# Optimization experiments

Measured on AMD Instinct MI355X. Metric: run time of the kernel, lower is better.

## Reference

```python
import jax, jax.numpy as jnp
import numpy as np

D_MODEL = 1024
NUM_HEADS = 16


def setup_inputs() -> dict:
    key = jax.random.key(0)
    ks = jax.random.split(key, 5)
    std = float(np.sqrt(2.0 / (D_MODEL + D_MODEL)))
    def w(k):
        # approximate trunc_normal init with clipped normal (init only; math of fwd unaffected)
        v = jax.random.truncated_normal(k, -3.0, 3.0, (D_MODEL, D_MODEL), jnp.float32) * std
        return v
    x = jax.random.normal(ks[0], (4, 2048, D_MODEL), jnp.float32)
    return {
        "x": x,
        "wq": w(ks[1]),
        "wk": w(ks[2]),
        "wv": w(ks[3]),
        "wo": w(ks[4]),
    }


def reference(x, wq, wk, wv, wo):
    b, s, d = x.shape
    h = NUM_HEADS
    dk = d // h
    # Linear: einsum('o i, ... i -> ... o')
    def proj(w):
        y = jnp.einsum('oi,bsi->bso', w, x)
        return y.reshape(b, s, h, dk).transpose(0, 2, 1, 3)  # b h s dk
    Q, K, V = proj(wq), proj(wk), proj(wv)
    scale = 1.0 / jnp.sqrt(jnp.asarray(dk, x.dtype))
    scores = jnp.einsum('bhqd,bhkd->bhqk', Q, K) * scale
    mask = jnp.tril(jnp.ones((s, s), dtype=bool))
    scores = jnp.where(mask, scores, -jnp.inf)
    attn = jax.nn.softmax(scores, axis=-1)
    out = jnp.einsum('bhqk,bhkd->bhqd', attn, V)
    out = out.transpose(0, 2, 1, 3).reshape(b, s, d)
    return jnp.einsum('oi,bsi->bso', wo, out)
```

## Files before the change

### kernel.cpp

```cpp
#include <hip/hip_runtime.h>
#include <hip/hip_bf16.h>


typedef __bf16 bf16x8 __attribute__((ext_vector_type(8)));
typedef __bf16 bf16x4 __attribute__((ext_vector_type(4)));
typedef float  f32x4  __attribute__((ext_vector_type(4)));
typedef float  f32x16 __attribute__((ext_vector_type(16)));
typedef unsigned int u32x4_t __attribute__((ext_vector_type(4)));

#define GLOBAL_AS __attribute__((address_space(1)))
#define LDS_AS    __attribute__((address_space(3)))

__device__ __forceinline__ void gload16(const void* g, void* l) {
    __builtin_amdgcn_global_load_lds((const GLOBAL_AS void*)g, (LDS_AS void*)l, 16, 0, 0);
}

__device__ __forceinline__ unsigned int cvtpk_bf16(float lo, float hi) {
    unsigned int r;
    asm("v_cvt_pk_bf16_f32 %0, %1, %2" : "=v"(r) : "v"(lo), "v"(hi));
    return r;
}

#define WAITVM4 asm volatile("s_waitcnt vmcnt(4)" ::: "memory")
#define WAITVM0 asm volatile("s_waitcnt vmcnt(0)" ::: "memory")
#define WAITLGKM0 asm volatile("s_waitcnt lgkmcnt(0)" ::: "memory")
#define SCHEDB  __builtin_amdgcn_sched_barrier(0)

__global__ __launch_bounds__(256) void cast_kernel(
    const float* __restrict__ x, const float* __restrict__ wq,
    const float* __restrict__ wk, const float* __restrict__ wv,
    const float* __restrict__ wo, __bf16* __restrict__ xb, __bf16* __restrict__ wb) {
    int bid = blockIdx.x;
    const float* src; __bf16* dst; int base;
    if (bid < 4096) {
        src = x; dst = xb; base = bid * 2048;
    } else {
        int r = bid - 4096; int wi = r >> 9;
        src = (wi == 0) ? wq : (wi == 1) ? wk : (wi == 2) ? wv : wo;
        dst = wb + wi * 1048576; base = (r & 511) * 2048;
    }
    int idx = base + threadIdx.x * 8;
    float4 a = *(const float4*)(src + idx);
    float4 b = *(const float4*)(src + idx + 4);
    bf16x8 o;
    o[0] = (__bf16)a.x; o[1] = (__bf16)a.y; o[2] = (__bf16)a.z; o[3] = (__bf16)a.w;
    o[4] = (__bf16)b.x; o[5] = (__bf16)b.y; o[6] = (__bf16)b.z; o[7] = (__bf16)b.w;
    *(bf16x8*)(dst + idx) = o;
}

__global__ __launch_bounds__(512) void gemm_qkv_kernel(
    const __bf16* __restrict__ A, const __bf16* __restrict__ W,
    __bf16* __restrict__ Qb, __bf16* __restrict__ Kb, __bf16* __restrict__ Vt,
    float qscale) {
    __shared__ __align__(16) char lds[131072];
    const int t = threadIdx.x;
    const int wid = t >> 6, lane = t & 63;
    const int g = lane >> 4, m = lane & 15;
    const int wm = wid >> 2, wn = wid & 3;
    const int bid = (blockIdx.x & 7) * 48 + (blockIdx.x >> 3);
    const int mt = bid / 12, nt = bid % 12;
    const int m0 = mt * 256, n0 = nt * 256;
    const bool isV = (n0 >= 2048);

    const __bf16* aSrc[2][2]; int aDst[2][2];
    const __bf16* bSrc[2][2]; int bDst[2][2];
#pragma unroll
    for (int q = 0; q < 2; ++q) {
        const int j = t + q * 512;
        const int slot = j & 7;
        {
            const int r0 = (j >> 9) * 128 + ((j >> 3) & 63);
            aSrc[0][q] = A + (size_t)(m0 + r0) * 1024 + (slot ^ (r0 & 7)) * 8;
            aDst[0][q] = r0 * 128 + slot * 16;
            const int r1 = r0 + 64;
            aSrc[1][q] = A + (size_t)(m0 + r1) * 1024 + (slot ^ (r1 & 7)) * 8;
            aDst[1][q] = r1 * 128 + slot * 16;
        }
        {
            const int r0 = ((j >> 8) & 3) * 64 + ((j >> 3) & 31);
            bSrc[0][q] = W + (size_t)(n0 + r0) * 1024 + (slot ^ (r0 & 7)) * 8;
            bDst[0][q] = r0 * 128 + slot * 16;
            const int r1 = r0 + 32;
            bSrc[1][q] = W + (size_t)(n0 + r1) * 1024 + (slot ^ (r1 & 7)) * 8;
            bDst[1][q] = r1 * 128 + slot * 16;
        }
    }
    auto stageA = [&](int par, int kt, int d) {
        gload16(aSrc[par][0] + kt * 64, lds + d * 65536 + aDst[par][0]);
        gload16(aSrc[par][1] + kt * 64, lds + d * 65536 + aDst[par][1]);
    };
    auto stageB = [&](int par, int kt, int d) {
        gload16(bSrc[par][0] + kt * 64, lds + d * 65536 + 32768 + bDst[par][0]);
        gload16(bSrc[par][1] + kt * 64, lds + d * 65536 + 32768 + bDst[par][1]);
    };

    const int sw = (m & 7) << 4;
    const int offA0 = (wm * 128 + m) * 128 + ((g << 4) ^ sw);
    const int offB0 = (wn * 64 + m) * 128 + ((g << 4) ^ sw);

    stageA(0, 0, 0); stageA(1, 0, 0); stageB(0, 0, 0); stageB(1, 0, 0);
    stageA(0, 1, 1); stageB(0, 1, 1);
    WAITVM4;
    SCHEDB;
    __builtin_amdgcn_s_barrier();
    SCHEDB;

    f32x4 acc[8][4] = {};

#define QPHASE(MH, NH, STAGESTMT, POSTW)                                      \
    {                                                                         \
        const char* bA_ = lds + bufd * 65536;                                 \
        const char* bB_ = bA_ + 32768;                                        \
        bf16x8 af[4][2], bfr[2][2];                                           \
        _Pragma("unroll")                                                     \
        for (int i2 = 0; i2 < 4; ++i2) {                                      \
            const int off = offA0 + ((MH) * 4 + i2) * 2048;                   \
            af[i2][0] = *(const bf16x8*)(bA_ + off);                          \
            af[i2][1] = *(const bf16x8*)(bA_ + (off ^ 64));                   \
        }                                                                     \
        _Pragma("unroll")                                                     \
        for (int j2 = 0; j2 < 2; ++j2) {                                      \
            const int off = offB0 + ((NH) * 2 + j2) * 2048;                   \
            bfr[j2][0] = *(const bf16x8*)(bB_ + off);                         \
            bfr[j2][1] = *(const bf16x8*)(bB_ + (off ^ 64));                  \
        }                                                                     \
        STAGESTMT;                                                            \
        SCHEDB;                                                               \
        __builtin_amdgcn_s_barrier();                                         \
        WAITLGKM0; SCHEDB;                                                    \
        __builtin_amdgcn_s_setprio(1);                                        \
        if (isV) {                                                            \
            _Pragma("unroll")                                                 \
            for (int i2 = 0; i2 < 4; ++i2)                                    \
                _Pragma("unroll")                                             \
                for (int j2 = 0; j2 < 2; ++j2) {                              \
                    acc[(MH)*4+i2][(NH)*2+j2] = __builtin_amdgcn_mfma_f32_16x16x32_bf16( \
                        af[i2][0], bfr[j2][0], acc[(MH)*4+i2][(NH)*2+j2], 0, 0, 0);      \
                    acc[(MH)*4+i2][(NH)*2+j2] = __builtin_amdgcn_mfma_f32_16x16x32_bf16( \
                        af[i2][1], bfr[j2][1], acc[(MH)*4+i2][(NH)*2+j2], 0, 0, 0);      \
                }                                                             \
        } else {                                                              \
            _Pragma("unroll")                                                 \
            for (int i2 = 0; i2 < 4; ++i2)                                    \
                _Pragma("unroll")                                             \
                for (int j2 = 0; j2 < 2; ++j2) {                              \
                    acc[(MH)*4+i2][(NH)*2+j2] = __builtin_amdgcn_mfma_f32_16x16x32_bf16( \
                        bfr[j2][0], af[i2][0], acc[(MH)*4+i2][(NH)*2+j2], 0, 0, 0);      \
                    acc[(MH)*4+i2][(NH)*2+j2] = __builtin_amdgcn_mfma_f32_16x16x32_bf16( \
                        bfr[j2][1], af[i2][1], acc[(MH)*4+i2][(NH)*2+j2], 0, 0, 0);      \
                }                                                             \
        }                                                                     \
        __builtin_amdgcn_s_setprio(0);                                        \
        POSTW;                                                                \
        SCHEDB;                                                               \
        __builtin_amdgcn_s_barrier();                                         \
        SCHEDB;                                                               \
    }

    for (int kt = 0; kt < 16; ++kt) {
        const int bufd = kt & 1;
        const int nb = bufd ^ 1;
        QPHASE(0, 0, if (kt + 1 < 16) stageA(1, kt + 1, nb), );
        QPHASE(0, 1, if (kt + 1 < 16) stageB(1, kt + 1, nb), );
        QPHASE(1, 0, if (kt + 2 < 16) stageA(0, kt + 2, bufd), );
        if (kt < 14) {
            QPHASE(1, 1, stageB(0, kt + 2, bufd), WAITVM4);
        } else {
            QPHASE(1, 1, , WAITVM0);
        }
    }
#undef QPHASE

    if (isV) {
        const int bb = m0 >> 11;
        const int sb = (m0 & 2047) + wm * 128 + 4 * g;
        const int hbase = ((n0 - 2048) >> 6) + wn;
#pragma unroll
        for (int mi = 0; mi < 8; ++mi)
#pragma unroll
            for (int ni = 0; ni < 4; ++ni) {
                const int d = ni * 16 + m;
                bf16x4 pk;
                pk[0] = (__bf16)(acc[mi][ni][0]); pk[1] = (__bf16)(acc[mi][ni][1]);
                pk[2] = (__bf16)(acc[mi][ni][2]); pk[3] = (__bf16)(acc[mi][ni][3]);
                *(bf16x4*)(Vt + ((size_t)(bb * 16 + hbase) * 64 + d) * 2048 + sb + mi * 16) = pk;
            }
    } else {
        __bf16* C = (n0 < 1024) ? Qb : Kb;
        const float sc = (n0 < 1024) ? qscale : 1.f;
        const int cb = (n0 & 1023) + wn * 64 + 4 * g;
        const int row = m0 + wm * 128 + m;
#pragma unroll
        for (int mi = 0; mi < 8; ++mi)
#pragma unroll
            for (int ni = 0; ni < 4; ++ni) {
                bf16x4 pk;
                pk[0] = (__bf16)(acc[mi][ni][0] * sc); pk[1] = (__bf16)(acc[mi][ni][1] * sc);
                pk[2] = (__bf16)(acc[mi][ni][2] * sc); pk[3] = (__bf16)(acc[mi][ni][3] * sc);
                *(bf16x4*)(C + (size_t)(row + mi * 16) * 1024 + cb + ni * 16) = pk;
            }
    }
}

__global__ __launch_bounds__(256) void gemm_out_kernel(
    const __bf16* __restrict__ A, const __bf16* __restrict__ W, float* __restrict__ out) {
    __shared__ __align__(16) char lds[65536];
    const int t = threadIdx.x;
    const int wid = t >> 6, lane = t & 63;
    const int g = lane >> 4, m = lane & 15;
    const int wm = wid >> 1, wn = wid & 1;
    const int bid = (blockIdx.x & 7) * 64 + (blockIdx.x >> 3);
    const int mt = bid >> 3, nt = bid & 7;
    const int m0 = mt * 128, n0 = nt * 128;

    const __bf16* sA[4]; const __bf16* sB[4]; int dA[4];
#pragma unroll
    for (int i = 0; i < 4; ++i) {
        const int ci = i * 256 + t;
        const int row = ci >> 3;
        const int k8 = (ci & 7) ^ (row & 7);
        sA[i] = A + (size_t)(m0 + row) * 1024 + k8 * 8;
        sB[i] = W + (size_t)(n0 + row) * 1024 + k8 * 8;
        dA[i] = ci * 16;
    }
    auto stage = [&](int kt, char* buf) {
#pragma unroll
        for (int i = 0; i < 4; ++i) gload16(sA[i] + kt * 64, buf + dA[i]);
#pragma unroll
        for (int i = 0; i < 4; ++i) gload16(sB[i] + kt * 64, buf + 16384 + dA[i]);
    };

    const int sw = (m & 7) << 4;
    const int offA = (wm * 64 + m) * 128 + ((g << 4) ^ sw);
    const int offB = (wn * 64 + m) * 128 + ((g << 4) ^ sw);

    stage(0, lds);

    f32x4 acc[4][4] = {};
    for (int kt = 0; kt < 16; ++kt) {
        char* cbuf = lds + (kt & 1) * 32768;
        WAITVM0;
        SCHEDB;
        __builtin_amdgcn_s_barrier();
        SCHEDB;
        if (kt < 15) stage(kt + 1, lds + ((kt + 1) & 1) * 32768);
        const char* bA = cbuf;
        const char* bB = cbuf + 16384;
        bf16x8 a0[4], b0[4], a1[4], b1[4];
#pragma unroll
        for (int i = 0; i < 4; ++i) {
            a0[i] = *(const bf16x8*)(bA + (offA + i * 2048));
            b0[i] = *(const bf16x8*)(bB + (offB + i * 2048));
            a1[i] = *(const bf16x8*)(bA + ((offA + i * 2048) ^ 64));
            b1[i] = *(const bf16x8*)(bB + ((offB + i * 2048) ^ 64));
        }
        __builtin_amdgcn_s_setprio(1);
#pragma unroll
        for (int mi = 0; mi < 4; ++mi)
#pragma unroll
            for (int ni = 0; ni < 4; ++ni)
                acc[mi][ni] = __builtin_amdgcn_mfma_f32_16x16x32_bf16(b0[ni], a0[mi], acc[mi][ni], 0, 0, 0);
#pragma unroll
        for (int mi = 0; mi < 4; ++mi)
#pragma unroll
            for (int ni = 0; ni < 4; ++ni)
                acc[mi][ni] = __builtin_amdgcn_mfma_f32_16x16x32_bf16(b1[ni], a1[mi], acc[mi][ni], 0, 0, 0);
        __builtin_amdgcn_s_setprio(0);
    }

    const int row = m0 + wm * 64 + m;
    const int col = n0 + wn * 64 + 4 * g;
#pragma unroll
    for (int mi = 0; mi < 4; ++mi)
#pragma unroll
        for (int ni = 0; ni < 4; ++ni)
            *(f32x4*)(out + (size_t)(row + mi * 16) * 1024 + col + ni * 16) = acc[mi][ni];
}

__global__ __launch_bounds__(128, 2) void attn_kernel(
    const __bf16* __restrict__ Qb, const __bf16* __restrict__ Kb,
    const __bf16* __restrict__ Vt, __bf16* __restrict__ Ob) {
    __shared__ __align__(16) char lds[32768];
    const int t = threadIdx.x;
    const int w = t >> 6, lane = t & 63;
    const int l31 = lane & 31, hi = lane >> 5;
    const int qb = (blockIdx.x >> 3) & 15;
    const int bh = (blockIdx.x & 7) | ((blockIdx.x >> 7) << 3);
    const size_t sbase = (size_t)(bh >> 4) * 2048;
    const int hoff = (bh & 15) * 64;

    const char* Kbase = (const char*)Kb + (sbase * 1024 + hoff) * 2;
    const char* Vbase = (const char*)Vt + (size_t)bh * 262144;
    const int srow = lane >> 3;
    const int scol = ((lane & 7) ^ srow) << 4;
    const int sw = (l31 & 7) << 4;
    int colx[4];
#pragma unroll
    for (int i = 0; i < 4; ++i) colx[i] = (32 * i + 16 * hi) ^ sw;

    auto stage = [&](int kv0, char* lK) {
        char* lV = lK + 8192;
#pragma unroll
        for (int i = 0; i < 4; ++i) {
            const int chunk = i * 2 + w;
            const int row = chunk * 8 + srow;
            gload16(Kbase + (size_t)(kv0 + row) * 2048 + scol, lK + chunk * 1024);
            gload16(Vbase + (size_t)row * 4096 + (size_t)kv0 * 2 + scol, lV + chunk * 1024);
        }
    };

    const int q0A = qb * 64 + w * 32;
    const int q0B = (31 - qb) * 64 + w * 32;
    const int qA = q0A + l31, qB = q0B + l31;
    const int nstream = 32 - qb;

    const __bf16* qrowA = Qb + (sbase + q0A + l31) * 1024 + hoff + 8 * hi;
    const __bf16* qrowB = Qb + (sbase + q0B + l31) * 1024 + hoff + 8 * hi;
    bf16x8 qfA[4], qfB[4];
#pragma unroll
    for (int cq = 0; cq < 4; ++cq) {
        qfA[cq] = *(const bf16x8*)(qrowA + 16 * cq);
        qfB[cq] = *(const bf16x8*)(qrowB + 16 * cq);
    }

    f32x16 oA0 = {}, oA1 = {}, oB0 = {}, oB1 = {};
    float mA = -__builtin_inff(), lA = 0.f;
    float mB = -__builtin_inff(), lB = 0.f;

    auto process = [&](const f32x16& s0r, const f32x16& s1r, int qq, bool diag,
                       int kv0, float& mrun, float& lrun, f32x16& o0, f32x16& o1,
                       const char* lV) {
        float pp[32];
#pragma unroll
        for (int rr = 0; rr < 16; ++rr) { pp[rr] = s0r[rr]; pp[16 + rr] = s1r[rr]; }
        if (diag) {
#pragma unroll
            for (int rr = 0; rr < 16; ++rr) {
                const int kvl = (rr & 3) + 8 * (rr >> 2) + 4 * hi;
                if (kv0 + kvl > qq)      pp[rr]      = -__builtin_inff();
                if (kv0 + 32 + kvl > qq) pp[16 + rr] = -__builtin_inff();
            }
        }
        float m8[8];
#pragma unroll
        for (int i = 0; i < 8; ++i)
            m8[i] = fmaxf(fmaxf(pp[4 * i], pp[4 * i + 1]), fmaxf(pp[4 * i + 2], pp[4 * i + 3]));
        float tmax = fmaxf(fmaxf(fmaxf(m8[0], m8[1]), fmaxf(m8[2], m8[3])),
                           fmaxf(fmaxf(m8[4], m8[5]), fmaxf(m8[6], m8[7])));
        const bool skip = __all(tmax <= mrun + 8.f);
        if (!skip) {
            float tq = fmaxf(tmax, __shfl_xor(tmax, 32));
            float mnew = fmaxf(mrun, tq);
            float al = __builtin_amdgcn_exp2f(mrun - mnew);
            lrun *= al;
#pragma unroll
            for (int rr = 0; rr < 16; ++rr) { o0[rr] *= al; o1[rr] *= al; }
            mrun = mnew;
        }
#pragma unroll
        for (int rr = 0; rr < 32; ++rr) pp[rr] = __builtin_amdgcn_exp2f(pp[rr] - mrun);
        float s8[8];
#pragma unroll
        for (int i = 0; i < 8; ++i)
            s8[i] = (pp[4 * i] + pp[4 * i + 1]) + (pp[4 * i + 2] + pp[4 * i + 3]);
        float rsum = ((s8[0] + s8[1]) + (s8[2] + s8[3])) + ((s8[4] + s8[5]) + (s8[6] + s8[7]));
        rsum += __shfl_xor(rsum, 32);
        lrun += rsum;

        __builtin_amdgcn_s_setprio(1);
#pragma unroll
        for (int cc = 0; cc < 4; ++cc) {
            const int pb = cc * 8;
            unsigned int A0 = cvtpk_bf16(pp[pb + 0], pp[pb + 1]);
            unsigned int A1 = cvtpk_bf16(pp[pb + 2], pp[pb + 3]);
            unsigned int B0 = cvtpk_bf16(pp[pb + 4], pp[pb + 5]);
            unsigned int B1 = cvtpk_bf16(pp[pb + 6], pp[pb + 7]);
            asm("v_permlane32_swap_b32 %0, %1" : "+v"(A0), "+v"(B0));
            asm("v_permlane32_swap_b32 %0, %1" : "+v"(A1), "+v"(B1));
            u32x4_t wvv; wvv[0] = A0; wvv[1] = A1; wvv[2] = B0; wvv[3] = B1;
            bf16x8 pa = __builtin_bit_cast(bf16x8, wvv);
            const int vcol = (32 * cc + 16 * hi) ^ sw;
            bf16x8 v0 = *(const bf16x8*)(lV + l31 * 128 + vcol);
            bf16x8 v1 = *(const bf16x8*)(lV + (l31 + 32) * 128 + vcol);
            o0 = __builtin_amdgcn_mfma_f32_32x32x16_bf16(v0, pa, o0, 0, 0, 0);
            o1 = __builtin_amdgcn_mfma_f32_32x32x16_bf16(v1, pa, o1, 0, 0, 0);
        }
        __builtin_amdgcn_s_setprio(0);
    };

    stage(0, lds);

    for (int tt = 0; tt < nstream; ++tt) {
        const int cur = tt & 1;
        char* lcur = lds + cur * 16384;
        WAITVM0;
        SCHEDB;
        __builtin_amdgcn_s_barrier();
        SCHEDB;
        if (tt + 1 < nstream) stage((tt + 1) * 64, lds + (cur ^ 1) * 16384);

        const int kv0 = tt * 64;
        const char* lK = lcur;
        const char* lV = lcur + 8192;
        const bool dual = (tt <= qb);

        f32x16 sA0 = {}, sA1 = {}, sB0 = {}, sB1 = {};
        __builtin_amdgcn_s_setprio(1);
        if (dual) {
#pragma unroll
            for (int cc = 0; cc < 4; ++cc) {
                bf16x8 k0 = *(const bf16x8*)(lK + l31 * 128 + colx[cc]);
                bf16x8 k1 = *(const bf16x8*)(lK + (l31 + 32) * 128 + colx[cc]);
                sA0 = __builtin_amdgcn_mfma_f32_32x32x16_bf16(k0, qfA[cc], sA0, 0, 0, 0);
                sA1 = __builtin_amdgcn_mfma_f32_32x32x16_bf16(k1, qfA[cc], sA1, 0, 0, 0);
                sB0 = __builtin_amdgcn_mfma_f32_32x32x16_bf16(k0, qfB[cc], sB0, 0, 0, 0);
                sB1 = __builtin_amdgcn_mfma_f32_32x32x16_bf16(k1, qfB[cc], sB1, 0, 0, 0);
            }
        } else {
#pragma unroll
            for (int cc = 0; cc < 4; ++cc) {
                bf16x8 k0 = *(const bf16x8*)(lK + l31 * 128 + colx[cc]);
                bf16x8 k1 = *(const bf16x8*)(lK + (l31 + 32) * 128 + colx[cc]);
                sB0 = __builtin_amdgcn_mfma_f32_32x32x16_bf16(k0, qfB[cc], sB0, 0, 0, 0);
                sB1 = __builtin_amdgcn_mfma_f32_32x32x16_bf16(k1, qfB[cc], sB1, 0, 0, 0);
            }
        }
        __builtin_amdgcn_s_setprio(0);

        if (dual)
            process(sA0, sA1, qA, tt == qb, kv0, mA, lA, oA0, oA1, lV);
        process(sB0, sB1, qB, tt == nstream - 1, kv0, mB, lB, oB0, oB1, lV);
    }

    {
        const float inv = 1.f / lA;
        __bf16* orow = Ob + (sbase + q0A + l31) * 1024 + hoff;
#pragma unroll
        for (int rq = 0; rq < 4; ++rq) {
            bf16x4 e0, e1;
#pragma unroll
            for (int jj = 0; jj < 4; ++jj) {
                e0[jj] = (__bf16)(oA0[rq * 4 + jj] * inv);
                e1[jj] = (__bf16)(oA1[rq * 4 + jj] * inv);
            }
            *(bf16x4*)(orow + 4 * hi + 8 * rq) = e0;
            *(bf16x4*)(orow + 32 + 4 * hi + 8 * rq) = e1;
        }
    }
    {
        const float inv = 1.f / lB;
        __bf16* orow = Ob + (sbase + q0B + l31) * 1024 + hoff;
#pragma unroll
        for (int rq = 0; rq < 4; ++rq) {
            bf16x4 e0, e1;
#pragma unroll
            for (int jj = 0; jj < 4; ++jj) {
                e0[jj] = (__bf16)(oB0[rq * 4 + jj] * inv);
                e1[jj] = (__bf16)(oB1[rq * 4 + jj] * inv);
            }
            *(bf16x4*)(orow + 4 * hi + 8 * rq) = e0;
            *(bf16x4*)(orow + 32 + 4 * hi + 8 * rq) = e1;
        }
    }
}

extern "C" void kernel_launch(void* const* d_in, const int* in_sizes, int n_in,
                              void* d_out, int out_size, void* d_ws, size_t ws_size,
                              hipStream_t stream) {
    const float* x  = (const float*)d_in[0];
    const float* wq = (const float*)d_in[1];
    const float* wk = (const float*)d_in[2];
    const float* wv = (const float*)d_in[3];
    const float* wo = (const float*)d_in[4];

    char* ws = (char*)d_ws;
    __bf16* xb = (__bf16*)(ws);
    __bf16* wb = (__bf16*)(ws + 16777216);
    __bf16* Qb = (__bf16*)(ws + 25165824);
    __bf16* Kb = (__bf16*)(ws + 41943040);
    __bf16* Vt = (__bf16*)(ws + 58720256);
    __bf16* Ob = (__bf16*)(ws + 75497472);

    const float qscale = 0.18033688011112043f;

    cast_kernel<<<6144, 256, 0, stream>>>(x, wq, wk, wv, wo, xb, wb);
    gemm_qkv_kernel<<<384, 512, 0, stream>>>(xb, wb, Qb, Kb, Vt, qscale);
    attn_kernel<<<1024, 128, 0, stream>>>(Qb, Kb, Vt, Ob);
    gemm_out_kernel<<<512, 256, 0, stream>>>(Ob, wb + 3145728, (float*)d_out);
}
```

Measured before the change: 195.4 us.

## Merge four quarter-phases per k-tile into two half-phases with fewer barriers

Restructures the QKV projection GEMM main loop from four quarter-tile phases, each with two barriers, into two half-tile phases. The B fragments are loaded once per k-tile and reused across both M halves. The next-stage A and B loads are issued together per phase, which halves barrier count and cuts redundant LDS reads of B. In exchange, more fragments are held in registers at once, and there are fewer interleaving points for global loads. The race safety of staging into the current buffer now depends on the single mid-iteration barrier.

```diff
diff --git a/kernel.cpp b/kernel.cpp
--- a/kernel.cpp
+++ b/kernel.cpp
@@ -107,69 +107,91 @@
 
     f32x4 acc[8][4] = {};
 
-#define QPHASE(MH, NH, STAGESTMT, POSTW)                                      \
-    {                                                                         \
-        const char* bA_ = lds + bufd * 65536;                                 \
-        const char* bB_ = bA_ + 32768;                                        \
-        bf16x8 af[4][2], bfr[2][2];                                           \
-        _Pragma("unroll")                                                     \
-        for (int i2 = 0; i2 < 4; ++i2) {                                      \
-            const int off = offA0 + ((MH) * 4 + i2) * 2048;                   \
-            af[i2][0] = *(const bf16x8*)(bA_ + off);                          \
-            af[i2][1] = *(const bf16x8*)(bA_ + (off ^ 64));                   \
-        }                                                                     \
-        _Pragma("unroll")                                                     \
-        for (int j2 = 0; j2 < 2; ++j2) {                                      \
-            const int off = offB0 + ((NH) * 2 + j2) * 2048;                   \
-            bfr[j2][0] = *(const bf16x8*)(bB_ + off);                         \
-            bfr[j2][1] = *(const bf16x8*)(bB_ + (off ^ 64));                  \
-        }                                                                     \
-        STAGESTMT;                                                            \
-        SCHEDB;                                                               \
-        __builtin_amdgcn_s_barrier();                                         \
-        WAITLGKM0; SCHEDB;                                                    \
-        __builtin_amdgcn_s_setprio(1);                                        \
-        if (isV) {                                                            \
-            _Pragma("unroll")                                                 \
-            for (int i2 = 0; i2 < 4; ++i2)                                    \
-                _Pragma("unroll")                                             \
-                for (int j2 = 0; j2 < 2; ++j2) {                              \
-                    acc[(MH)*4+i2][(NH)*2+j2] = __builtin_amdgcn_mfma_f32_16x16x32_bf16( \
-                        af[i2][0], bfr[j2][0], acc[(MH)*4+i2][(NH)*2+j2], 0, 0, 0);      \
-                    acc[(MH)*4+i2][(NH)*2+j2] = __builtin_amdgcn_mfma_f32_16x16x32_bf16( \
-                        af[i2][1], bfr[j2][1], acc[(MH)*4+i2][(NH)*2+j2], 0, 0, 0);      \
-                }                                                             \
-        } else {                                                              \
-            _Pragma("unroll")                                                 \
-            for (int i2 = 0; i2 < 4; ++i2)                                    \
-                _Pragma("unroll")                                             \
-                for (int j2 = 0; j2 < 2; ++j2) {                              \
-                    acc[(MH)*4+i2][(NH)*2+j2] = __builtin_amdgcn_mfma_f32_16x16x32_bf16( \
-                        bfr[j2][0], af[i2][0], acc[(MH)*4+i2][(NH)*2+j2], 0, 0, 0);      \
-                    acc[(MH)*4+i2][(NH)*2+j2] = __builtin_amdgcn_mfma_f32_16x16x32_bf16( \
-                        bfr[j2][1], af[i2][1], acc[(MH)*4+i2][(NH)*2+j2], 0, 0, 0);      \
-                }                                                             \
-        }                                                                     \
-        __builtin_amdgcn_s_setprio(0);                                        \
-        POSTW;                                                                \
-        SCHEDB;                                                               \
-        __builtin_amdgcn_s_barrier();                                         \
-        SCHEDB;                                                               \
-    }
-
     for (int kt = 0; kt < 16; ++kt) {
         const int bufd = kt & 1;
         const int nb = bufd ^ 1;
-        QPHASE(0, 0, if (kt + 1 < 16) stageA(1, kt + 1, nb), );
-        QPHASE(0, 1, if (kt + 1 < 16) stageB(1, kt + 1, nb), );
-        QPHASE(1, 0, if (kt + 2 < 16) stageA(0, kt + 2, bufd), );
-        if (kt < 14) {
-            QPHASE(1, 1, stageB(0, kt + 2, bufd), WAITVM4);
+        const char* bA_ = lds + bufd * 65536;
+        const char* bB_ = bA_ + 32768;
+
+        bf16x8 bf[4][2], af[4][2];
+#pragma unroll
+        for (int j2 = 0; j2 < 4; ++j2) {
+            const int off = offB0 + j2 * 2048;
+            bf[j2][0] = *(const bf16x8*)(bB_ + off);
+            bf[j2][1] = *(const bf16x8*)(bB_ + (off ^ 64));
+        }
+#pragma unroll
+        for (int i2 = 0; i2 < 4; ++i2) {
+            const int off = offA0 + i2 * 2048;
+            af[i2][0] = *(const bf16x8*)(bA_ + off);
+            af[i2][1] = *(const bf16x8*)(bA_ + (off ^ 64));
+        }
+        if (kt + 1 < 16) { stageA(1, kt + 1, nb); stageB(1, kt + 1, nb); }
+        WAITLGKM0; SCHEDB;
+        __builtin_amdgcn_s_setprio(1);
+        if (isV) {
+#pragma unroll
+            for (int i2 = 0; i2 < 4; ++i2)
+#pragma unroll
+                for (int j2 = 0; j2 < 4; ++j2) {
+                    acc[i2][j2] = __builtin_amdgcn_mfma_f32_16x16x32_bf16(
+                        af[i2][0], bf[j2][0], acc[i2][j2], 0, 0, 0);
+                    acc[i2][j2] = __builtin_amdgcn_mfma_f32_16x16x32_bf16(
+                        af[i2][1], bf[j2][1], acc[i2][j2], 0, 0, 0);
+                }
         } else {
-            QPHASE(1, 1, , WAITVM0);
-        }
-    }
-#undef QPHASE
+#pragma unroll
+            for (int i2 = 0; i2 < 4; ++i2)
+#pragma unroll
+                for (int j2 = 0; j2 < 4; ++j2) {
+                    acc[i2][j2] = __builtin_amdgcn_mfma_f32_16x16x32_bf16(
+                        bf[j2][0], af[i2][0], acc[i2][j2], 0, 0, 0);
+                    acc[i2][j2] = __builtin_amdgcn_mfma_f32_16x16x32_bf16(
+                        bf[j2][1], af[i2][1], acc[i2][j2], 0, 0, 0);
+                }
+        }
+        __builtin_amdgcn_s_setprio(0);
+        SCHEDB;
+        __builtin_amdgcn_s_barrier();
+        SCHEDB;
+
+        bf16x8 ah[4][2];
+#pragma unroll
+        for (int i2 = 0; i2 < 4; ++i2) {
+            const int off = offA0 + (4 + i2) * 2048;
+            ah[i2][0] = *(const bf16x8*)(bA_ + off);
+            ah[i2][1] = *(const bf16x8*)(bA_ + (off ^ 64));
+        }
+        if (kt + 2 < 16) { stageA(0, kt + 2, bufd); stageB(0, kt + 2, bufd); }
+        WAITLGKM0; SCHEDB;
+        __builtin_amdgcn_s_setprio(1);
+        if (isV) {
+#pragma unroll
+            for (int i2 = 0; i2 < 4; ++i2)
+#pragma unroll
+                for (int j2 = 0; j2 < 4; ++j2) {
+                    acc[4 + i2][j2] = __builtin_amdgcn_mfma_f32_16x16x32_bf16(
+                        ah[i2][0], bf[j2][0], acc[4 + i2][j2], 0, 0, 0);
+                    acc[4 + i2][j2] = __builtin_amdgcn_mfma_f32_16x16x32_bf16(
+                        ah[i2][1], bf[j2][1], acc[4 + i2][j2], 0, 0, 0);
+                }
+        } else {
+#pragma unroll
+            for (int i2 = 0; i2 < 4; ++i2)
+#pragma unroll
+                for (int j2 = 0; j2 < 4; ++j2) {
+                    acc[4 + i2][j2] = __builtin_amdgcn_mfma_f32_16x16x32_bf16(
+                        bf[j2][0], ah[i2][0], acc[4 + i2][j2], 0, 0, 0);
+                    acc[4 + i2][j2] = __builtin_amdgcn_mfma_f32_16x16x32_bf16(
+                        bf[j2][1], ah[i2][1], acc[4 + i2][j2], 0, 0, 0);
+                }
+        }
+        __builtin_amdgcn_s_setprio(0);
+        if (kt < 14) { WAITVM4; } else { WAITVM0; }
+        SCHEDB;
+        __builtin_amdgcn_s_barrier();
+        SCHEDB;
+    }
 
     if (isV) {
         const int bb = m0 >> 11;
```

Result: slower. 265.4 us (+35.8%).
